# Optimization experiments

Measured on AMD Instinct MI355X. Metric: run time of the kernel, lower is better.

## Reference

```python
import jax, jax.numpy as jnp
import numpy as np

B, CIN, COUT, H, W = 16, 512, 128, 64, 64


def setup_inputs() -> dict:
    key = jax.random.key(0)
    k1, k2, k3 = jax.random.split(key, 3)
    x = jax.random.normal(k1, (B, CIN, H, W), dtype=jnp.float32)
    style = jax.random.normal(k2, (B, CIN), dtype=jnp.float32)
    # kaiming_normal_ on [COUT, CIN, 1, 1]: fan_in = CIN*1*1, std = sqrt(2/fan_in)
    weight = jax.random.normal(k3, (COUT, CIN), dtype=jnp.float32) * np.float32(np.sqrt(2.0 / CIN))
    return {"x": x, "style": style, "weight": weight}


def reference(x, style, weight):
    # Per-sample modulated weight: mw[b,o,c] = style[b,c] * weight[o,c]
    # 1x1 conv, padding=0, stride=1 -> batched channel-mixing GEMM:
    # out[b,o,h,w] = sum_c mw[b,o,c] * x[b,c,h,w]
    return jnp.einsum('oc,bc,bchw->bohw', weight, style, x)
```

## Files before the change

### kernel.cpp

```cpp
#include <hip/hip_runtime.h>
#include <stdint.h>

#define NB    16
#define CIN   512
#define COUT  128
#define HW    4096
#define BN    128
#define BK    32
#define NIT   (CIN / BK)

using bf16x8  = __attribute__((ext_vector_type(8))) __bf16;
using floatx4 = __attribute__((ext_vector_type(4))) float;

__device__ __forceinline__ unsigned short f2bf_bits(float f) {
    union { float f; unsigned u; } v; v.f = f;
    return (unsigned short)((v.u + 0x7fffu + ((v.u >> 16) & 1u)) >> 16);
}

#define GLD16(g, l)                                                            \
    __builtin_amdgcn_global_load_lds(                                          \
        (const __attribute__((address_space(1))) void*)(g),                    \
        (__attribute__((address_space(3))) void*)(l), 16, 0, 0)

__global__ __launch_bounds__(256)
void modw_kernel(const float* __restrict__ style,
                 const float* __restrict__ weight,
                 __bf16* __restrict__ mw)
{
    const int id = blockIdx.x * 256 + threadIdx.x;
    const int k8 = id & 63;
    const int m  = (id >> 6) & 127;
    const int b  = id >> 13;

    const float4 w0 = *(const float4*)(weight + m * CIN + k8 * 8);
    const float4 w1 = *(const float4*)(weight + m * CIN + k8 * 8 + 4);
    const float4 s0 = *(const float4*)(style + b * CIN + k8 * 8);
    const float4 s1 = *(const float4*)(style + b * CIN + k8 * 8 + 4);

    union { unsigned short us[8]; bf16x8 v; } pk;
    pk.us[0] = f2bf_bits(w0.x * s0.x);
    pk.us[1] = f2bf_bits(w0.y * s0.y);
    pk.us[2] = f2bf_bits(w0.z * s0.z);
    pk.us[3] = f2bf_bits(w0.w * s0.w);
    pk.us[4] = f2bf_bits(w1.x * s1.x);
    pk.us[5] = f2bf_bits(w1.y * s1.y);
    pk.us[6] = f2bf_bits(w1.z * s1.z);
    pk.us[7] = f2bf_bits(w1.w * s1.w);
    *(bf16x8*)(mw + ((size_t)(b * 64 + k8) * 128 + m) * 8) = pk.v;
}

__global__ __launch_bounds__(512, 4)
void modconv1x1_kernel(const float* __restrict__ x,
                       const __bf16* __restrict__ mw,
                       float* __restrict__ out)
{
    __shared__ __align__(16) __bf16 Alds[2][4096];
    __shared__ __align__(16) float  Blds[2][BK * BN];

    const int tid  = threadIdx.x;
    const int lane = tid & 63;
    const int wave = tid >> 6;
    const int quad = lane >> 4;
    const int l15  = lane & 15;

    const int b  = blockIdx.x >> 5;
    const int n0 = (blockIdx.x & 31) * BN;

    const char*  xbb  = (const char*)(x + (size_t)b * CIN * HW + n0);
    float*       outb = out + (size_t)b * COUT * HW + n0;
    const char*  mwb  = (const char*)mw + (size_t)b * (64 * 128 * 16);

    const int wm = (wave & 1) * 64;
    const int wn = (wave >> 1) * 32;

    const int brsel = lane >> 5;
    const int bcol  = lane & 31;

    floatx4 acc[4][2];
    #pragma unroll
    for (int i = 0; i < 4; ++i)
        #pragma unroll
        for (int j = 0; j < 2; ++j)
            acc[i][j] = (floatx4){0.f, 0.f, 0.f, 0.f};

#define STAGE(K0, BUF)                                                         \
    {                                                                          \
        const char* at = mwb + (size_t)(K0) * 256;                             \
        char*       al = (char*)&Alds[BUF][0];                                 \
        GLD16(at + wave * 1024 + lane * 16, al + wave * 1024);                 \
        char* bl = (char*)&Blds[BUF][0];                                       \
        _Pragma("unroll")                                                      \
        for (int g = 0; g < 2; ++g) {                                          \
            const int gi = wave * 2 + g;                            \
            const int r  = gi * 2 + brsel;                      \
            GLD16(xbb + (size_t)((K0) + r) * (HW * 4) + bcol * 16,             \
                  bl + gi * 1024);                                             \
        }                                                                      \
    }

    STAGE(0, 0)

    int cur = 0;
    for (int it = 0; it < NIT; ++it) {
        __syncthreads();

        if (it + 1 < NIT) STAGE((it + 1) * BK, cur ^ 1)

        bf16x8 af[4];
        #pragma unroll
        for (int tm = 0; tm < 4; ++tm)
            af[tm] = *(const bf16x8*)&Alds[cur][(quad * COUT + wm + tm * 16 + l15) * 8];

        bf16x8 bfr[2];
        #pragma unroll
        for (int tn = 0; tn < 2; ++tn) {
            union { unsigned short us[8]; bf16x8 v; } pk;
            #pragma unroll
            for (int j = 0; j < 8; ++j)
                pk.us[j] = f2bf_bits(Blds[cur][(quad * 8 + j) * BN + wn + tn * 16 + l15]);
            bfr[tn] = pk.v;
        }

        #pragma unroll
        for (int tm = 0; tm < 4; ++tm)
            #pragma unroll
            for (int tn = 0; tn < 2; ++tn)
                acc[tm][tn] = __builtin_amdgcn_mfma_f32_16x16x32_bf16(
                    af[tm], bfr[tn], acc[tm][tn], 0, 0, 0);

        cur ^= 1;
    }
#undef STAGE

    #pragma unroll
    for (int tm = 0; tm < 4; ++tm) {
        const int o = wm + tm * 16 + quad * 4;
        #pragma unroll
        for (int tn = 0; tn < 2; ++tn) {
            const int n = wn + tn * 16 + l15;
            #pragma unroll
            for (int r = 0; r < 4; ++r)
                outb[(size_t)(o + r) * HW + n] = acc[tm][tn][r];
        }
    }
}

extern "C" void kernel_launch(void* const* d_in, const int* in_sizes, int n_in,
                              void* d_out, int out_size, void* d_ws, size_t ws_size,
                              hipStream_t stream) {
    const float* x      = (const float*)d_in[0];
    const float* style  = (const float*)d_in[1];
    const float* weight = (const float*)d_in[2];
    float* out = (float*)d_out;
    __bf16* mw = (__bf16*)d_ws;

    modw_kernel<<<dim3(512), dim3(256), 0, stream>>>(style, weight, mw);
    modconv1x1_kernel<<<dim3(NB * 32), dim3(512), 0, stream>>>(x, mw, out);
}
```

Baseline: 206.9 us.

## Replace LDS-staged GEMM with register-direct loads and per-wave 16-column tiles

The conv kernel drops shared-memory staging and block barriers. Each wave now loads its x fragment straight from global memory into registers, double-buffered across k-steps, and reads the modulated weights directly from global/L2. Each wave computes all 128 output channels for 16 columns, and blocks shrink to 256 threads with twice as many blocks, interleaved across batches. This removes LDS round trips and syncs, at the cost of scalar 4-byte strided global loads for x and repeated reads of the weights by every wave.

```diff
diff --git a/kernel.cpp b/kernel.cpp
--- a/kernel.cpp
+++ b/kernel.cpp
@@ -5,9 +5,6 @@
 #define CIN   512
 #define COUT  128
 #define HW    4096
-#define BN    128
-#define BK    32
-#define NIT   (CIN / BK)
 
 using bf16x8  = __attribute__((ext_vector_type(8))) __bf16;
 using floatx4 = __attribute__((ext_vector_type(4))) float;
@@ -16,11 +13,6 @@
     union { float f; unsigned u; } v; v.f = f;
     return (unsigned short)((v.u + 0x7fffu + ((v.u >> 16) & 1u)) >> 16);
 }
-
-#define GLD16(g, l)                                                            \
-    __builtin_amdgcn_global_load_lds(                                          \
-        (const __attribute__((address_space(1))) void*)(g),                    \
-        (__attribute__((address_space(3))) void*)(l), 16, 0, 0)
 
 __global__ __launch_bounds__(256)
 void modw_kernel(const float* __restrict__ style,
@@ -49,99 +41,76 @@
     *(bf16x8*)(mw + ((size_t)(b * 64 + k8) * 128 + m) * 8) = pk.v;
 }
 
-__global__ __launch_bounds__(512, 4)
+__global__ __launch_bounds__(256, 4)
 void modconv1x1_kernel(const float* __restrict__ x,
                        const __bf16* __restrict__ mw,
                        float* __restrict__ out)
 {
-    __shared__ __align__(16) __bf16 Alds[2][4096];
-    __shared__ __align__(16) float  Blds[2][BK * BN];
-
     const int tid  = threadIdx.x;
     const int lane = tid & 63;
     const int wave = tid >> 6;
     const int quad = lane >> 4;
     const int l15  = lane & 15;
 
-    const int b  = blockIdx.x >> 5;
-    const int n0 = (blockIdx.x & 31) * BN;
+    const int b  = blockIdx.x & 15;
+    const int nt = blockIdx.x >> 4;
+    const int n0 = nt * 64 + wave * 16;
 
-    const char*  xbb  = (const char*)(x + (size_t)b * CIN * HW + n0);
-    float*       outb = out + (size_t)b * COUT * HW + n0;
-    const char*  mwb  = (const char*)mw + (size_t)b * (64 * 128 * 16);
+    const float*  xb  = x + (size_t)b * CIN * HW + (size_t)quad * 8 * HW + n0 + l15;
+    const __bf16* mwb = mw + (size_t)b * (64 * 128 * 8) + quad * (128 * 8) + l15 * 8;
+    float*        outb = out + (size_t)b * COUT * HW + n0 + l15;
 
-    const int wm = (wave & 1) * 64;
-    const int wn = (wave >> 1) * 32;
+    floatx4 acc[8];
+    #pragma unroll
+    for (int tm = 0; tm < 8; ++tm) acc[tm] = (floatx4){0.f, 0.f, 0.f, 0.f};
 
-    const int brsel = lane >> 5;
-    const int bcol  = lane & 31;
+    float xv0[8], xv1[8];
 
-    floatx4 acc[4][2];
-    #pragma unroll
-    for (int i = 0; i < 4; ++i)
-        #pragma unroll
-        for (int j = 0; j < 2; ++j)
-            acc[i][j] = (floatx4){0.f, 0.f, 0.f, 0.f};
+#define XLOAD(DST, IT)                                                        \
+    _Pragma("unroll")                                                         \
+    for (int j = 0; j < 8; ++j)                                               \
+        DST[j] = xb[((size_t)(IT) * 32 + j) * HW];
 
-#define STAGE(K0, BUF)                                                         \
-    {                                                                          \
-        const char* at = mwb + (size_t)(K0) * 256;                             \
-        char*       al = (char*)&Alds[BUF][0];                                 \
-        GLD16(at + wave * 1024 + lane * 16, al + wave * 1024);                 \
-        char* bl = (char*)&Blds[BUF][0];                                       \
-        _Pragma("unroll")                                                      \
-        for (int g = 0; g < 2; ++g) {                                          \
-            const int gi = wave * 2 + g;                            \
-            const int r  = gi * 2 + brsel;                      \
-            GLD16(xbb + (size_t)((K0) + r) * (HW * 4) + bcol * 16,             \
-                  bl + gi * 1024);                                             \
-        }                                                                      \
+#define BODY(IT, CUR, NXT, PRE)                                               \
+    {                                                                         \
+        if (PRE) { XLOAD(NXT, (IT) + 1) }                                     \
+        const __bf16* ap = mwb + (size_t)(IT) * (4 * 128 * 8);                \
+        bf16x8 af0[4], af1[4];                                                \
+        _Pragma("unroll")                                                     \
+        for (int tm = 0; tm < 4; ++tm)                                        \
+            af0[tm] = *(const bf16x8*)(ap + tm * (16 * 8));                   \
+        _Pragma("unroll")                                                     \
+        for (int tm = 0; tm < 4; ++tm)                                        \
+            af1[tm] = *(const bf16x8*)(ap + (4 + tm) * (16 * 8));             \
+        union { unsigned short us[8]; bf16x8 v; } pk;                         \
+        _Pragma("unroll")                                                     \
+        for (int j = 0; j < 8; ++j) pk.us[j] = f2bf_bits(CUR[j]);             \
+        _Pragma("unroll")                                                     \
+        for (int tm = 0; tm < 4; ++tm)                                        \
+            acc[tm] = __builtin_amdgcn_mfma_f32_16x16x32_bf16(                \
+                af0[tm], pk.v, acc[tm], 0, 0, 0);                             \
+        _Pragma("unroll")                                                     \
+        for (int tm = 0; tm < 4; ++tm)                                        \
+            acc[4 + tm] = __builtin_amdgcn_mfma_f32_16x16x32_bf16(            \
+                af1[tm], pk.v, acc[4 + tm], 0, 0, 0);                         \
     }
 
-    STAGE(0, 0)
-
-    int cur = 0;
-    for (int it = 0; it < NIT; ++it) {
-        __syncthreads();
-
-        if (it + 1 < NIT) STAGE((it + 1) * BK, cur ^ 1)
-
-        bf16x8 af[4];
-        #pragma unroll
-        for (int tm = 0; tm < 4; ++tm)
-            af[tm] = *(const bf16x8*)&Alds[cur][(quad * COUT + wm + tm * 16 + l15) * 8];
-
-        bf16x8 bfr[2];
-        #pragma unroll
-        for (int tn = 0; tn < 2; ++tn) {
-            union { unsigned short us[8]; bf16x8 v; } pk;
-            #pragma unroll
-            for (int j = 0; j < 8; ++j)
-                pk.us[j] = f2bf_bits(Blds[cur][(quad * 8 + j) * BN + wn + tn * 16 + l15]);
-            bfr[tn] = pk.v;
-        }
-
-        #pragma unroll
-        for (int tm = 0; tm < 4; ++tm)
-            #pragma unroll
-            for (int tn = 0; tn < 2; ++tn)
-                acc[tm][tn] = __builtin_amdgcn_mfma_f32_16x16x32_bf16(
-                    af[tm], bfr[tn], acc[tm][tn], 0, 0, 0);
-
-        cur ^= 1;
+    XLOAD(xv0, 0)
+    #pragma unroll 1
+    for (int it2 = 0; it2 < 8; ++it2) {
+        const int it = it2 * 2;
+        BODY(it,     xv0, xv1, 1)
+        BODY(it + 1, xv1, xv0, (it2 < 7))
     }
-#undef STAGE
+#undef BODY
+#undef XLOAD
 
     #pragma unroll
-    for (int tm = 0; tm < 4; ++tm) {
-        const int o = wm + tm * 16 + quad * 4;
+    for (int tm = 0; tm < 8; ++tm) {
+        const int o = tm * 16 + quad * 4;
         #pragma unroll
-        for (int tn = 0; tn < 2; ++tn) {
-            const int n = wn + tn * 16 + l15;
-            #pragma unroll
-            for (int r = 0; r < 4; ++r)
-                outb[(size_t)(o + r) * HW + n] = acc[tm][tn][r];
-        }
+        for (int r = 0; r < 4; ++r)
+            outb[(size_t)(o + r) * HW] = acc[tm][r];
     }
 }
 
@@ -155,5 +124,5 @@
     __bf16* mw = (__bf16*)d_ws;
 
     modw_kernel<<<dim3(512), dim3(256), 0, stream>>>(style, weight, mw);
-    modconv1x1_kernel<<<dim3(NB * 32), dim3(512), 0, stream>>>(x, mw, out);
+    modconv1x1_kernel<<<dim3(NB * 64), dim3(256), 0, stream>>>(x, mw, out);
 }
```

Result: slower. 218.9 us (+5.8%).

## Triple-buffer LDS staging with explicit vmcnt waits in the modulated conv GEMM

Applied to the files above, without the earlier changes.

Moves the main GEMM loop from double to triple buffering in LDS, so two K-tiles of global-to-LDS loads can be in flight while one tile is computed. Each iteration now waits with `s_waitcnt vmcnt(3)` plus a raw `s_barrier` instead of a full `__syncthreads`, and the last two tiles are handled in a peeled tail. This is meant to hide global load latency, which looks dominant given how far the kernel sits from bandwidth limits. The cost is more LDS per block (72KB instead of 48KB), which may cut resident blocks per CU, and it relies on the manual wait counts staying correct.

```diff
diff --git a/kernel.cpp b/kernel.cpp
--- a/kernel.cpp
+++ b/kernel.cpp
@@ -54,8 +54,8 @@
                        const __bf16* __restrict__ mw,
                        float* __restrict__ out)
 {
-    __shared__ __align__(16) __bf16 Alds[2][4096];
-    __shared__ __align__(16) float  Blds[2][BK * BN];
+    __shared__ __align__(16) __bf16 Alds[3][4096];
+    __shared__ __align__(16) float  Blds[3][BK * BN];
 
     const int tid  = threadIdx.x;
     const int lane = tid & 63;
@@ -98,39 +98,53 @@
         }                                                                      \
     }
 
+#define COMPUTE(BUF)                                                           \
+    {                                                                          \
+        bf16x8 af[4];                                                          \
+        _Pragma("unroll")                                                      \
+        for (int tm = 0; tm < 4; ++tm)                                         \
+            af[tm] = *(const bf16x8*)&Alds[BUF][(quad * COUT + wm + tm * 16 + l15) * 8]; \
+        bf16x8 bfr[2];                                                         \
+        _Pragma("unroll")                                                      \
+        for (int tn = 0; tn < 2; ++tn) {                                       \
+            union { unsigned short us[8]; bf16x8 v; } pk;                      \
+            _Pragma("unroll")                                                  \
+            for (int j = 0; j < 8; ++j)                                        \
+                pk.us[j] = f2bf_bits(Blds[BUF][(quad * 8 + j) * BN + wn + tn * 16 + l15]); \
+            bfr[tn] = pk.v;                                                    \
+        }                                                                      \
+        _Pragma("unroll")                                                      \
+        for (int tm = 0; tm < 4; ++tm)                                         \
+            _Pragma("unroll")                                                  \
+            for (int tn = 0; tn < 2; ++tn)                                     \
+                acc[tm][tn] = __builtin_amdgcn_mfma_f32_16x16x32_bf16(         \
+                    af[tm], bfr[tn], acc[tm][tn], 0, 0, 0);                    \
+    }
+
     STAGE(0, 0)
+    STAGE(BK, 1)
 
-    int cur = 0;
-    for (int it = 0; it < NIT; ++it) {
-        __syncthreads();
-
-        if (it + 1 < NIT) STAGE((it + 1) * BK, cur ^ 1)
-
-        bf16x8 af[4];
-        #pragma unroll
-        for (int tm = 0; tm < 4; ++tm)
-            af[tm] = *(const bf16x8*)&Alds[cur][(quad * COUT + wm + tm * 16 + l15) * 8];
-
-        bf16x8 bfr[2];
-        #pragma unroll
-        for (int tn = 0; tn < 2; ++tn) {
-            union { unsigned short us[8]; bf16x8 v; } pk;
-            #pragma unroll
-            for (int j = 0; j < 8; ++j)
-                pk.us[j] = f2bf_bits(Blds[cur][(quad * 8 + j) * BN + wn + tn * 16 + l15]);
-            bfr[tn] = pk.v;
-        }
-
-        #pragma unroll
-        for (int tm = 0; tm < 4; ++tm)
-            #pragma unroll
-            for (int tn = 0; tn < 2; ++tn)
-                acc[tm][tn] = __builtin_amdgcn_mfma_f32_16x16x32_bf16(
-                    af[tm], bfr[tn], acc[tm][tn], 0, 0, 0);
-
-        cur ^= 1;
+    int sc = 0;
+    int ss = 2;
+    int k0 = 2 * BK;
+    #pragma unroll 1
+    for (int it = 0; it < NIT - 2; ++it) {
+        asm volatile("s_waitcnt vmcnt(3)" ::: "memory");
+        __builtin_amdgcn_s_barrier();
+        STAGE(k0, ss)
+        COMPUTE(sc)
+        k0 += BK;
+        sc = (sc == 2) ? 0 : sc + 1;
+        ss = (ss == 2) ? 0 : ss + 1;
     }
+    asm volatile("s_waitcnt vmcnt(3)" ::: "memory");
+    __builtin_amdgcn_s_barrier();
+    COMPUTE(2)
+    asm volatile("s_waitcnt vmcnt(0)" ::: "memory");
+    __builtin_amdgcn_s_barrier();
+    COMPUTE(0)
 #undef STAGE
+#undef COMPUTE
 
     #pragma unroll
     for (int tm = 0; tm < 4; ++tm) {
```

Result: no change. 209.3 us (+1.2%).
